# Optimization experiments

Hardware: AMD Instinct MI355X
Metric: run time of the kernel (lower is better)

Reference implementation:

```python
import jax, jax.numpy as jnp
import numpy as np


def _conv(x, w, b, pad):
    y = jax.lax.conv_general_dilated(x, w, (1, 1), [(pad, pad), (pad, pad)],
                                     dimension_numbers=('NCHW', 'OIHW', 'NCHW'))
    return y + b[None, :, None, None]


def _leaky(x):
    return jnp.where(x >= 0, x, 0.2 * x)


def _up_nearest(t, s):
    return jnp.repeat(jnp.repeat(t, s, axis=2), s, axis=3)


def _to_plane(d, dx, dy, size):
    # nearest-upsample d,dx,dy by `size` and add per-subpixel plane offsets
    c = jnp.linspace(-(size - 1) / 2, (size - 1) / 2, size).astype(d.dtype)
    H, W = d.shape[2], d.shape[3]
    a = jnp.tile(c, W)[None, None, None, :]   # x-offset pattern along width
    b = jnp.tile(c, H)[None, None, :, None]   # y-offset pattern along height
    return _up_nearest(d, size) + a * _up_nearest(dx, size) + b * _up_nearest(dy, size)


def _warp(x, disp):
    # grid_sample(x, grid) with grid = (xx - disp, yy), align_corners=True, zero padding.
    # y coords are exact integers, so this reduces to 1-D linear interp along W.
    B, C, H, W = x.shape
    ix = jnp.arange(W, dtype=x.dtype)[None, None, :] - disp[:, 0]  # [B,H,W]
    x0 = jnp.floor(ix)
    wx = ix - x0
    x0i = x0.astype(jnp.int32)
    x1i = x0i + 1
    ok0 = ((x0i >= 0) & (x0i < W)).astype(x.dtype)
    ok1 = ((x1i >= 0) & (x1i < W)).astype(x.dtype)

    def gather(idx):
        idx = jnp.clip(idx, 0, W - 1)
        return jnp.take_along_axis(x, jnp.broadcast_to(idx[:, None], (B, C, H, W)), axis=3)

    return ((1 - wx) * ok0)[:, None] * gather(x0i) + (wx * ok1)[:, None] * gather(x1i)


def _unshuffle(x, r=4):
    B, C, H, W = x.shape
    return x.reshape(B, C, H // r, r, W // r, r).transpose(0, 1, 3, 5, 2, 4).reshape(B, C * r * r, H // r, W // r)


def _tile_warping(tile_plane, fea_l, fea_r):
    d, dx, dy = tile_plane[:, 0:1], tile_plane[:, 1:2], tile_plane[:, 2:3]
    cvs = []
    for k in (-1.0, 0.0, 1.0):
        local_d = _to_plane(d + k, dx, dy, 4)
        cv = jnp.sum(jnp.abs(fea_l - _warp(fea_r, local_d)), axis=1, keepdims=True)
        cvs.append(_unshuffle(cv, 4))
    return jnp.concatenate(cvs, axis=1)


def _upsample_hyp(h, scale=2.0, size=2):
    d = _to_plane(h[:, 0:1], h[:, 1:2], h[:, 2:3], size) * scale
    rest = _up_nearest(h[:, 1:], size)
    return jnp.concatenate([d, rest], axis=1)


def _forward(fea_l, fea_r, cur, prev,
             w_dec, b_dec, w0, b0,
             w_r0c1, b_r0c1, w_r0c2, b_r0c2,
             w_r1c1, b_r1c1, w_r1c2, b_r1c2,
             w_last, b_last):
    fea = _unshuffle(jnp.sum(jnp.abs(fea_l), axis=1, keepdims=True), 4)  # [B,16,H/4,W/4]

    cur_cv = _tile_warping(cur[:, :3], fea_l, fea_r)
    cur_cv = _leaky(_conv(jnp.concatenate([fea, cur_cv], 1), w_dec, b_dec, 0))

    up_prev = _upsample_hyp(prev, 2.0, 2)
    prev_cv = _tile_warping(up_prev[:, :3], fea_l, fea_r)
    prev_cv = _leaky(_conv(jnp.concatenate([fea, prev_cv], 1), w_dec, b_dec, 0))

    aug = jnp.concatenate([cur, cur_cv, up_prev, prev_cv], 1)  # 64 ch
    h = _leaky(_conv(aug, w0, b0, 0))
    # resblock0 (BasicBlock + outer LeakyReLU)
    t = _leaky(_conv(h, w_r0c1, b_r0c1, 1))
    h = _leaky(_conv(t, w_r0c2, b_r0c2, 1) + h)
    # resblock1
    t = _leaky(_conv(h, w_r1c1, b_r1c1, 1))
    h = _leaky(_conv(t, w_r1c2, b_r1c2, 1) + h)
    u = _conv(h, w_last, b_last, 1)  # 34 ch

    conf = u[:, :2]
    prev_delta = u[:, 2:18]
    cur_delta = u[:, 18:34]
    mask = jnp.argmax(conf, axis=1, keepdims=True).astype(u.dtype)

    upd_cur = cur + cur_delta
    upd_cur = jnp.concatenate([jax.nn.relu(upd_cur[:, :1]), upd_cur[:, 1:]], 1)
    upd_prev = up_prev + prev_delta
    upd_prev = jnp.concatenate([jax.nn.relu(upd_prev[:, :1]), upd_prev[:, 1:]], 1)

    refined = mask * upd_cur + (1 - mask) * upd_prev
    return (refined,
            jnp.concatenate([upd_cur, conf[:, 1:2]], 1),
            jnp.concatenate([upd_prev, conf[:, :1]], 1))


def setup_inputs() -> dict:
    key = jax.random.key(0)
    ks = jax.random.split(key, 16)
    B, C, H, W = 2, 16, 384, 1280
    Ht, Wt = H // 4, W // 4
    inp = {
        'fea_l': jax.random.normal(ks[0], (B, C, H, W), jnp.float32),
        'fea_r': jax.random.normal(ks[1], (B, C, H, W), jnp.float32),
        'current_hypothesis': jax.random.uniform(ks[2], (B, 16, Ht, Wt), jnp.float32) * 4.0,
        'prev_hypothesis': jax.random.uniform(ks[3], (B, 16, Ht // 2, Wt // 2), jnp.float32) * 4.0,
    }
    s = 0.05
    inp['w_dec'] = jax.random.normal(ks[4], (16, 64, 1, 1), jnp.float32) * s
    inp['b_dec'] = jax.random.normal(ks[5], (16,), jnp.float32) * s
    inp['w0'] = jax.random.normal(ks[6], (32, 64, 1, 1), jnp.float32) * s
    inp['b0'] = jax.random.normal(ks[7], (32,), jnp.float32) * s
    inp['w_r0c1'] = jax.random.normal(ks[8], (32, 32, 3, 3), jnp.float32) * s
    inp['b_r0c1'] = jax.random.normal(ks[9], (32,), jnp.float32) * s
    inp['w_r0c2'] = jax.random.normal(ks[10], (32, 32, 3, 3), jnp.float32) * s
    inp['b_r0c2'] = jax.random.normal(ks[11], (32,), jnp.float32) * s
    inp['w_r1c1'] = jax.random.normal(ks[12], (32, 32, 3, 3), jnp.float32) * s
    inp['b_r1c1'] = jax.random.normal(ks[13], (32,), jnp.float32) * s
    inp['w_r1c2'] = jax.random.normal(ks[14], (32, 32, 3, 3), jnp.float32) * s
    inp['b_r1c2'] = jax.random.normal(ks[15], (32,), jnp.float32) * s
    k2 = jax.random.split(jax.random.key(1), 2)
    inp['w_last'] = jax.random.normal(k2[0], (34, 32, 3, 3), jnp.float32) * s
    inp['b_last'] = jax.random.normal(k2[1], (34,), jnp.float32) * s
    return inp


def reference(fea_l, fea_r, current_hypothesis, prev_hypothesis,
              w_dec, b_dec, w0, b0,
              w_r0c1, b_r0c1, w_r0c2, b_r0c2,
              w_r1c1, b_r1c1, w_r1c2, b_r1c2,
              w_last, b_last):
    return _forward(fea_l, fea_r, current_hypothesis, prev_hypothesis,
                    w_dec, b_dec, w0, b0,
                    w_r0c1, b_r0c1, w_r0c2, b_r0c2,
                    w_r1c1, b_r1c1, w_r1c2, b_r1c2,
                    w_last, b_last)
```

## Files before the change

kernel.cpp:

```cpp
#include <hip/hip_runtime.h>
#include <hip/hip_bf16.h>

#define B_ 2
#define C_ 16
#define H_ 384
#define W_ 1280
#define HT_ 96
#define WT_ 320
#define SP_ (HT_*WT_)
#define NPIX_ (B_*SP_)
#define HP_ 48
#define WP_ 160
#define SPP_ (HP_*WP_)

__device__ __forceinline__ float leaky(float v){ return v >= 0.f ? v : 0.2f*v; }

__global__ __launch_bounds__(256) void k_sentinel(float* __restrict__ out, int n, float v){
    int i = blockIdx.x*256 + threadIdx.x;
    if (i < n) out[i] = v;
}

__global__ __launch_bounds__(256) void k_warpfused(const float* __restrict__ cur,
        const float* __restrict__ prev,
        const float* __restrict__ fl, const float* __restrict__ fr,
        const float* __restrict__ wdec, const float* __restrict__ bdec,
        const float* __restrict__ w0, const float* __restrict__ b0,
        float* __restrict__ h){
    __shared__ float vc[16][65];
    __shared__ float vp[16][49];
    __shared__ float wl[64][16];
    __shared__ float inb[16][65];
    __shared__ float w0l[64][33];
    __shared__ float bl0[32];
    int tid = threadIdx.x;
    for (int i = tid; i < 1024; i += 256) wl[i>>4][i&15] = wdec[(i&15)*64 + (i>>4)];
    for (int i = tid; i < 2048; i += 256) w0l[i>>5][i&31] = w0[(i&31)*64 + (i>>5)];
    if (tid < 32) bl0[tid] = b0[tid];

    int tp  = tid >> 4;
    int sub = tid & 15;
    int yy = sub >> 2, xx = sub & 3;
    int ty = blockIdx.y;
    int tx0 = blockIdx.x*16;
    int tx = tx0 + tp;
    int b  = blockIdx.z;
    int y = ty*4 + yy, x = tx*4 + xx;

    {
        int ch = tid >> 4, px = tid & 15;
        int txp = tx0 + px;
        inb[px][ch] = cur[((size_t)(b*16 + ch)*HT_ + ty)*WT_ + txp];
        size_t pbase = ((size_t)(b*16)*HP_ + (ty>>1))*WP_ + (txp>>1);
        float v;
        if (ch == 0){
            float dv  = prev[pbase];
            float dxv = prev[pbase + SPP_];
            float dyv = prev[pbase + 2*SPP_];
            float cxs = (txp & 1) ? 0.5f : -0.5f;
            float cys = (ty  & 1) ? 0.5f : -0.5f;
            v = (dv + cxs*dxv + cys*dyv) * 2.0f;
        } else {
            v = prev[pbase + (size_t)ch*SPP_];
        }
        inb[px][32 + ch] = v;
    }

    size_t cb = ((size_t)(b*16)*HT_ + ty)*WT_ + tx;
    float dC  = cur[cb];
    float dxC = cur[cb + SP_];
    float dyC = cur[cb + 2*SP_];
    size_t pb = ((size_t)(b*16)*HP_ + (ty>>1))*WP_ + (tx>>1);
    float pd  = prev[pb];
    float pdx = prev[pb + SPP_];
    float pdy = prev[pb + 2*SPP_];
    float cxs = (tx & 1) ? 0.5f : -0.5f;
    float cys = (ty & 1) ? 0.5f : -0.5f;
    float dP  = (pd + cxs*pdx + cys*pdy) * 2.0f;

    const float c4[4] = {-1.5f,-0.5f,0.5f,1.5f};
    float ld0C = dC + c4[xx]*dxC + c4[yy]*dyC;
    float ld0P = dP + c4[xx]*pdx + c4[yy]*pdy;

    float wloC[4], whiC[4]; int xcC[4];
    {
        float ix  = (float)x - ld0C;
        float x0f = floorf(ix);
        float wx  = ix - x0f;
        int   x0  = (int)x0f;
        #pragma unroll
        for (int j = 0; j < 4; j++){
            int xi = x0 + (j-1);
            bool ok = (xi >= 0) && (xi < W_);
            xcC[j]  = xi < 0 ? 0 : (xi > W_-1 ? W_-1 : xi);
            wloC[j] = ok ? (1.f - wx) : 0.f;
            whiC[j] = ok ? wx : 0.f;
        }
    }
    float wloP[4], whiP[4]; int xcP[4];
    {
        float ix  = (float)x - ld0P;
        float x0f = floorf(ix);
        float wx  = ix - x0f;
        int   x0  = (int)x0f;
        #pragma unroll
        for (int j = 0; j < 4; j++){
            int xi = x0 + (j-1);
            bool ok = (xi >= 0) && (xi < W_);
            xcP[j]  = xi < 0 ? 0 : (xi > W_-1 ? W_-1 : xi);
            wloP[j] = ok ? (1.f - wx) : 0.f;
            whiP[j] = ok ? wx : 0.f;
        }
    }
    const float* plc = fl + (size_t)(b*C_)*H_*W_ + (size_t)y*W_ + x;
    const float* prr = fr + (size_t)(b*C_)*H_*W_ + (size_t)y*W_;
    float fsum=0.f, s0C=0.f, s1C=0.f, s2C=0.f, s0P=0.f, s1P=0.f, s2P=0.f;
    #pragma unroll 4
    for (int c = 0; c < C_; c++){
        const float* prc = prr + (size_t)c*H_*W_;
        float a  = plc[(size_t)c*H_*W_];
        float c0 = prc[xcC[0]];
        float c1 = prc[xcC[1]];
        float c2 = prc[xcC[2]];
        float c3 = prc[xcC[3]];
        float p0 = prc[xcP[0]];
        float p1 = prc[xcP[1]];
        float p2 = prc[xcP[2]];
        float p3 = prc[xcP[3]];
        fsum += fabsf(a);
        s0C += fabsf(a - (wloC[2]*c2 + whiC[3]*c3));
        s1C += fabsf(a - (wloC[1]*c1 + whiC[2]*c2));
        s2C += fabsf(a - (wloC[0]*c0 + whiC[1]*c1));
        s0P += fabsf(a - (wloP[2]*p2 + whiP[3]*p3));
        s1P += fabsf(a - (wloP[1]*p1 + whiP[2]*p2));
        s2P += fabsf(a - (wloP[0]*p0 + whiP[1]*p1));
    }
    vc[tp][sub]      = fsum;
    vc[tp][16 + sub] = s0C;
    vc[tp][32 + sub] = s1C;
    vc[tp][48 + sub] = s2C;
    vp[tp][sub]      = s0P;
    vp[tp][16 + sub] = s1P;
    vp[tp][32 + sub] = s2P;
    __syncthreads();

    {
        int oc  = tid >> 4;
        int tp2 = tid & 15;
        float common = 0.f, aC = 0.f, aP = 0.f;
        #pragma unroll 8
        for (int ic = 0; ic < 16; ic++) common += vc[tp2][ic] * wl[ic][oc];
        #pragma unroll 8
        for (int ic = 16; ic < 64; ic++){
            aC += vc[tp2][ic]      * wl[ic][oc];
            aP += vp[tp2][ic - 16] * wl[ic][oc];
        }
        float bb = bdec[oc];
        inb[tp2][16 + oc] = leaky(common + aC + bb);
        inb[tp2][48 + oc] = leaky(common + aP + bb);
    }
    __syncthreads();

    {
        int og = tid >> 4;
        int px = tid & 15;
        float acc0 = bl0[og];
        float acc1 = bl0[og + 16];
        #pragma unroll 8
        for (int ic = 0; ic < 64; ic++){
            float v = inb[px][ic];
            acc0 += v * w0l[ic][og];
            acc1 += v * w0l[ic][og + 16];
        }
        size_t hb = ((size_t)(b*32 + og)*HT_ + ty)*WT_ + tx0 + px;
        h[hb]              = leaky(acc0);
        h[hb + (size_t)16*HT_*WT_] = leaky(acc1);
    }
}

template<bool RES>
__global__ __launch_bounds__(256) void k_conv3(const float* __restrict__ in,
        const float* __restrict__ w, const float* __restrict__ bias,
        const float* res, float* out){
    __shared__ float it[8][6][34];
    __shared__ float wl[8][9][16];
    int tid = threadIdx.x;
    int gx = blockIdx.x*32, gy = blockIdx.y*4;
    int b     = blockIdx.z >> 1;
    int ocsel = blockIdx.z & 1;
    int ocg  = tid >> 6;
    int slot = tid & 63;
    int tx2  = (slot & 15)*2;
    int ty   = slot >> 4;
    float acc[4][2];
    #pragma unroll
    for (int o = 0; o < 4; o++)
        #pragma unroll
        for (int p = 0; p < 2; p++) acc[o][p] = 0.f;

    for (int ic0 = 0; ic0 < 32; ic0 += 8){
        for (int i = tid; i < 8*6*34; i += 256){
            int ic = i/(6*34); int r = i - ic*(6*34);
            int iy = r/34;     int ixx = r - iy*34;
            int ggy = gy + iy - 1, ggx = gx + ixx - 1;
            float v = 0.f;
            if (ggy >= 0 && ggy < HT_ && ggx >= 0 && ggx < WT_)
                v = in[((size_t)(b*32 + ic0+ic)*HT_ + ggy)*WT_ + ggx];
            it[ic][iy][ixx] = v;
        }
        for (int i = tid; i < 1152; i += 256){
            int ic = i/144; int r = i - ic*144;
            int kk = r >> 4; int ocl = r & 15;
            wl[ic][kk][ocl] = w[(size_t)((ocsel*16 + ocl)*32 + ic0+ic)*9 + kk];
        }
        __syncthreads();
        #pragma unroll
        for (int ic = 0; ic < 8; ic++){
            #pragma unroll
            for (int dy = 0; dy < 3; dy++){
                float inr[4];
                #pragma unroll
                for (int j = 0; j < 4; j++) inr[j] = it[ic][ty+dy][tx2+j];
                #pragma unroll
                for (int dx = 0; dx < 3; dx++){
                    const float4 wv = *(const float4*)(&wl[ic][dy*3+dx][ocg*4]);
                    const float wa[4] = {wv.x, wv.y, wv.z, wv.w};
                    #pragma unroll
                    for (int o = 0; o < 4; o++)
                        #pragma unroll
                        for (int p = 0; p < 2; p++)
                            acc[o][p] += inr[dx+p]*wa[o];
                }
            }
        }
        __syncthreads();
    }
    int oc0 = ocsel*16 + ocg*4;
    int yo = gy + ty;
    #pragma unroll
    for (int o = 0; o < 4; o++){
        float bo = bias[oc0+o];
        size_t ob = ((size_t)(b*32 + oc0+o)*HT_ + yo)*WT_ + gx + tx2;
        #pragma unroll
        for (int p = 0; p < 2; p++){
            float v = acc[o][p] + bo;
            if (RES) v += res[ob+p];
            out[ob+p] = leaky(v);
        }
    }
}

__global__ __launch_bounds__(256) void k_last(const float* __restrict__ in,
        const float* __restrict__ w, const float* __restrict__ bias,
        const float* __restrict__ cur, const float* __restrict__ prev,
        float* __restrict__ out){
    __shared__ float it[8][10][34];
    __shared__ float wl[8][9][36];
    __shared__ float bl[34];
    int tid = threadIdx.x;
    int gx = blockIdx.x*32, gy = blockIdx.y*8;
    int b = blockIdx.z;
    int tx = tid & 31, ty = tid >> 5;
    if (tid < 34) bl[tid] = bias[tid];
    float acc[34];
    #pragma unroll
    for (int o = 0; o < 34; o++) acc[o] = 0.f;

    for (int ic0 = 0; ic0 < 32; ic0 += 8){
        for (int i = tid; i < 8*10*34; i += 256){
            int ic = i/340; int r = i - ic*340;
            int iy = r/34;  int ixx = r - iy*34;
            int ggy = gy + iy - 1, ggx = gx + ixx - 1;
            float v = 0.f;
            if (ggy >= 0 && ggy < HT_ && ggx >= 0 && ggx < WT_)
                v = in[((size_t)(b*32 + ic0+ic)*HT_ + ggy)*WT_ + ggx];
            it[ic][iy][ixx] = v;
        }
        for (int i = tid; i < 8*9*34; i += 256){
            int ic = i/306; int r = i - ic*306;
            int kk = r/34;  int oc = r - kk*34;
            wl[ic][kk][oc] = w[(size_t)(oc*32 + ic0+ic)*9 + kk];
        }
        __syncthreads();
        for (int ic = 0; ic < 8; ic++){
            #pragma unroll
            for (int dy = 0; dy < 3; dy++){
                const float vv[3] = { it[ic][ty+dy][tx], it[ic][ty+dy][tx+1], it[ic][ty+dy][tx+2] };
                #pragma unroll
                for (int dx = 0; dx < 3; dx++){
                    const float* wp = &wl[ic][dy*3+dx][0];
                    float v = vv[dx];
                    #pragma unroll
                    for (int o = 0; o < 34; o++) acc[o] += v*wp[o];
                }
            }
        }
        __syncthreads();
    }
    int x = gx + tx, y = gy + ty;
    size_t pix = (size_t)y*WT_ + x;
    float conf0 = acc[0] + bl[0];
    float conf1 = acc[1] + bl[1];
    bool m = conf1 > conf0;
    size_t src = ((size_t)(b*16)*HP_ + (y>>1))*WP_ + (x>>1);
    float cx = (x & 1) ? 0.5f : -0.5f;
    float cy = (y & 1) ? 0.5f : -0.5f;
    const float* cp = cur + (size_t)b*16*SP_ + pix;
    float* o0 = out +               (size_t)b*16*SP_ + pix;
    float* o1 = out +  983040u  +   (size_t)b*17*SP_ + pix;
    float* o2 = out + 2027520u  +   (size_t)b*17*SP_ + pix;
    #pragma unroll
    for (int c = 0; c < 16; c++){
        float upv;
        if (c == 0){
            float dv  = prev[src];
            float dxv = prev[src + SPP_];
            float dyv = prev[src + 2*SPP_];
            upv = (dv + cx*dxv + cy*dyv) * 2.0f;
        } else {
            upv = prev[src + (size_t)c*SPP_];
        }
        float ucv = cp[(size_t)c*SP_] + acc[18+c] + bl[18+c];
        upv = upv + acc[2+c] + bl[2+c];
        if (c == 0){ ucv = fmaxf(ucv, 0.f); upv = fmaxf(upv, 0.f); }
        float rf = m ? ucv : upv;
        o0[(size_t)c*SP_] = rf;
        o1[(size_t)c*SP_] = ucv;
        o2[(size_t)c*SP_] = upv;
    }
    o1[(size_t)16*SP_] = conf1;
    o2[(size_t)16*SP_] = conf0;
}

#define WS_NEED (32u*NPIX_*4u)
#define OUT_ELEMS 3072000

extern "C" void kernel_launch(void* const* d_in, const int* in_sizes, int n_in,
                              void* d_out, int out_size, void* d_ws, size_t ws_size,
                              hipStream_t stream) {
    const float* fea_l  = (const float*)d_in[0];
    const float* fea_r  = (const float*)d_in[1];
    const float* cur    = (const float*)d_in[2];
    const float* prev   = (const float*)d_in[3];
    const float* w_dec  = (const float*)d_in[4];
    const float* b_dec  = (const float*)d_in[5];
    const float* w0     = (const float*)d_in[6];
    const float* b0     = (const float*)d_in[7];
    const float* w_r0c1 = (const float*)d_in[8];
    const float* b_r0c1 = (const float*)d_in[9];
    const float* w_r0c2 = (const float*)d_in[10];
    const float* b_r0c2 = (const float*)d_in[11];
    const float* w_r1c1 = (const float*)d_in[12];
    const float* b_r1c1 = (const float*)d_in[13];
    const float* w_r1c2 = (const float*)d_in[14];
    const float* b_r1c2 = (const float*)d_in[15];
    const float* w_last = (const float*)d_in[16];
    const float* b_last = (const float*)d_in[17];

    float* out = (float*)d_out;

    if (ws_size < (size_t)WS_NEED){
        k_sentinel<<<(OUT_ELEMS+255)/256, 256, 0, stream>>>(out, OUT_ELEMS, (float)(ws_size >> 10));
        return;
    }

    float* h = (float*)d_ws;
    float* t = out;

    dim3 gw(20, 96, 2);
    k_warpfused<<<gw, 256, 0, stream>>>(cur, prev, fea_l, fea_r, w_dec, b_dec, w0, b0, h);

    dim3 g3(10, 24, 4);
    k_conv3<false><<<g3, 256, 0, stream>>>(h, w_r0c1, b_r0c1, nullptr, t);
    k_conv3<true> <<<g3, 256, 0, stream>>>(t, w_r0c2, b_r0c2, h, h);
    k_conv3<false><<<g3, 256, 0, stream>>>(h, w_r1c1, b_r1c1, nullptr, t);
    k_conv3<true> <<<g3, 256, 0, stream>>>(t, w_r1c2, b_r1c2, h, h);

    dim3 gl(10, 12, 2);
    k_last<<<gl, 256, 0, stream>>>(h, w_last, b_last, cur, prev, out);
}
```

Baseline: 453.7 us.

## Stage right-feature rows in LDS for warp cost volume and double-buffer conv tiles

The fused warp kernel computes the block's min/max gather column with shared-memory atomics. When that span fits in 256 columns, it stages the needed fl/fr rows into a shared-memory pool in groups of 4 channels instead of doing scattered global gathers per channel. The weight and input loads for the decoder are moved after the cost loop so they can reuse the same pool. The conv3 and last-conv kernels switch to double-buffered shared tiles, with the row pitch padded to 35, so the next channel group loads while the current one computes. This adds shared memory, more synchronisation, and a fallback path for wide spans.

```diff
diff --git a/kernel.cpp b/kernel.cpp
--- a/kernel.cpp
+++ b/kernel.cpp
@@ -28,15 +28,16 @@
         float* __restrict__ h){
     __shared__ float vc[16][65];
     __shared__ float vp[16][49];
-    __shared__ float wl[64][16];
-    __shared__ float inb[16][65];
-    __shared__ float w0l[64][33];
-    __shared__ float bl0[32];
+    __shared__ int   s_red[2];
+    __shared__ float upool[5152];
+    float (*flA)[4][65]  = (float(*)[4][65])(upool);
+    float (*frW)[4][257] = (float(*)[4][257])(upool + 1040);
+    float (*wlp)[16]     = (float(*)[16])(upool);
+    float (*inb)[65]     = (float(*)[65])(upool + 1024);
+    float (*w0l)[33]     = (float(*)[33])(upool + 2064);
+    float *bl0           = upool + 4176;
+
     int tid = threadIdx.x;
-    for (int i = tid; i < 1024; i += 256) wl[i>>4][i&15] = wdec[(i&15)*64 + (i>>4)];
-    for (int i = tid; i < 2048; i += 256) w0l[i>>5][i&31] = w0[(i&31)*64 + (i>>5)];
-    if (tid < 32) bl0[tid] = b0[tid];
-
     int tp  = tid >> 4;
     int sub = tid & 15;
     int yy = sub >> 2, xx = sub & 3;
@@ -46,24 +47,7 @@
     int b  = blockIdx.z;
     int y = ty*4 + yy, x = tx*4 + xx;
 
-    {
-        int ch = tid >> 4, px = tid & 15;
-        int txp = tx0 + px;
-        inb[px][ch] = cur[((size_t)(b*16 + ch)*HT_ + ty)*WT_ + txp];
-        size_t pbase = ((size_t)(b*16)*HP_ + (ty>>1))*WP_ + (txp>>1);
-        float v;
-        if (ch == 0){
-            float dv  = prev[pbase];
-            float dxv = prev[pbase + SPP_];
-            float dyv = prev[pbase + 2*SPP_];
-            float cxs = (txp & 1) ? 0.5f : -0.5f;
-            float cys = (ty  & 1) ? 0.5f : -0.5f;
-            v = (dv + cxs*dxv + cys*dyv) * 2.0f;
-        } else {
-            v = prev[pbase + (size_t)ch*SPP_];
-        }
-        inb[px][32 + ch] = v;
-    }
+    if (tid == 0){ s_red[0] = 0x7fffffff; s_red[1] = -0x7fffffff; }
 
     size_t cb = ((size_t)(b*16)*HT_ + ty)*WT_ + tx;
     float dC  = cur[cb];
@@ -111,29 +95,79 @@
             whiP[j] = ok ? wx : 0.f;
         }
     }
-    const float* plc = fl + (size_t)(b*C_)*H_*W_ + (size_t)y*W_ + x;
-    const float* prr = fr + (size_t)(b*C_)*H_*W_ + (size_t)y*W_;
+    __syncthreads();
+    atomicMin(&s_red[0], min(xcC[0], xcP[0]));
+    atomicMax(&s_red[1], max(xcC[3], xcP[3]));
+    __syncthreads();
+    int wmn   = s_red[0];
+    int wspan = s_red[1] - wmn + 1;
+
+    const size_t HW = (size_t)H_*W_;
     float fsum=0.f, s0C=0.f, s1C=0.f, s2C=0.f, s0P=0.f, s1P=0.f, s2P=0.f;
-    #pragma unroll 4
-    for (int c = 0; c < C_; c++){
-        const float* prc = prr + (size_t)c*H_*W_;
-        float a  = plc[(size_t)c*H_*W_];
-        float c0 = prc[xcC[0]];
-        float c1 = prc[xcC[1]];
-        float c2 = prc[xcC[2]];
-        float c3 = prc[xcC[3]];
-        float p0 = prc[xcP[0]];
-        float p1 = prc[xcP[1]];
-        float p2 = prc[xcP[2]];
-        float p3 = prc[xcP[3]];
-        fsum += fabsf(a);
-        s0C += fabsf(a - (wloC[2]*c2 + whiC[3]*c3));
-        s1C += fabsf(a - (wloC[1]*c1 + whiC[2]*c2));
-        s2C += fabsf(a - (wloC[0]*c0 + whiC[1]*c1));
-        s0P += fabsf(a - (wloP[2]*p2 + whiP[3]*p3));
-        s1P += fabsf(a - (wloP[1]*p1 + whiP[2]*p2));
-        s2P += fabsf(a - (wloP[0]*p0 + whiP[1]*p1));
-    }
+
+    if (wspan <= 256){
+        int W64 = (wspan + 63) & ~63;
+        int o0C = xcC[0]-wmn, o1C = xcC[1]-wmn, o2C = xcC[2]-wmn, o3C = xcC[3]-wmn;
+        int o0P = xcP[0]-wmn, o1P = xcP[1]-wmn, o2P = xcP[2]-wmn, o3P = xcP[3]-wmn;
+        int y0 = ty*4, xb = tx0*4;
+        int pxl = tp*4 + xx;
+        for (int c0 = 0; c0 < 16; c0 += 4){
+            for (int i = tid; i < 1024; i += 256){
+                int ci = i >> 8, r = (i >> 6) & 3, px = i & 63;
+                flA[ci][r][px] = fl[(size_t)(b*C_ + c0+ci)*HW + (size_t)(y0+r)*W_ + xb + px];
+            }
+            for (int ci = 0; ci < 4; ci++){
+                const float* base = fr + (size_t)(b*C_ + c0+ci)*HW;
+                for (int r = 0; r < 4; r++){
+                    const float* rowp = base + (size_t)(y0+r)*W_;
+                    for (int px = tid; px < W64; px += 256){
+                        int gx = wmn + px;
+                        frW[ci][r][px] = (gx < W_) ? rowp[gx] : 0.f;
+                    }
+                }
+            }
+            __syncthreads();
+            #pragma unroll
+            for (int ci = 0; ci < 4; ci++){
+                float a = flA[ci][yy][pxl];
+                const float* row = &frW[ci][yy][0];
+                float c0v = row[o0C], c1v = row[o1C], c2v = row[o2C], c3v = row[o3C];
+                float p0v = row[o0P], p1v = row[o1P], p2v = row[o2P], p3v = row[o3P];
+                fsum += fabsf(a);
+                s0C += fabsf(a - (wloC[2]*c2v + whiC[3]*c3v));
+                s1C += fabsf(a - (wloC[1]*c1v + whiC[2]*c2v));
+                s2C += fabsf(a - (wloC[0]*c0v + whiC[1]*c1v));
+                s0P += fabsf(a - (wloP[2]*p2v + whiP[3]*p3v));
+                s1P += fabsf(a - (wloP[1]*p1v + whiP[2]*p2v));
+                s2P += fabsf(a - (wloP[0]*p0v + whiP[1]*p1v));
+            }
+            __syncthreads();
+        }
+    } else {
+        const float* plc = fl + (size_t)(b*C_)*HW + (size_t)y*W_ + x;
+        const float* prr = fr + (size_t)(b*C_)*HW + (size_t)y*W_;
+        #pragma unroll 4
+        for (int c = 0; c < C_; c++){
+            const float* prc = prr + (size_t)c*HW;
+            float a  = plc[(size_t)c*HW];
+            float c0v = prc[xcC[0]];
+            float c1v = prc[xcC[1]];
+            float c2v = prc[xcC[2]];
+            float c3v = prc[xcC[3]];
+            float p0v = prc[xcP[0]];
+            float p1v = prc[xcP[1]];
+            float p2v = prc[xcP[2]];
+            float p3v = prc[xcP[3]];
+            fsum += fabsf(a);
+            s0C += fabsf(a - (wloC[2]*c2v + whiC[3]*c3v));
+            s1C += fabsf(a - (wloC[1]*c1v + whiC[2]*c2v));
+            s2C += fabsf(a - (wloC[0]*c0v + whiC[1]*c1v));
+            s0P += fabsf(a - (wloP[2]*p2v + whiP[3]*p3v));
+            s1P += fabsf(a - (wloP[1]*p1v + whiP[2]*p2v));
+            s2P += fabsf(a - (wloP[0]*p0v + whiP[1]*p1v));
+        }
+    }
+
     vc[tp][sub]      = fsum;
     vc[tp][16 + sub] = s0C;
     vc[tp][32 + sub] = s1C;
@@ -141,6 +175,28 @@
     vp[tp][sub]      = s0P;
     vp[tp][16 + sub] = s1P;
     vp[tp][32 + sub] = s2P;
+
+    for (int i = tid; i < 1024; i += 256) wlp[i>>4][i&15] = wdec[(i&15)*64 + (i>>4)];
+    for (int i = tid; i < 2048; i += 256) w0l[i>>5][i&31] = w0[(i&31)*64 + (i>>5)];
+    if (tid < 32) bl0[tid] = b0[tid];
+    {
+        int ch = tid >> 4, px = tid & 15;
+        int txp = tx0 + px;
+        inb[px][ch] = cur[((size_t)(b*16 + ch)*HT_ + ty)*WT_ + txp];
+        size_t pbase = ((size_t)(b*16)*HP_ + (ty>>1))*WP_ + (txp>>1);
+        float v;
+        if (ch == 0){
+            float dv  = prev[pbase];
+            float dxv = prev[pbase + SPP_];
+            float dyv = prev[pbase + 2*SPP_];
+            float cx2 = (txp & 1) ? 0.5f : -0.5f;
+            float cy2 = (ty  & 1) ? 0.5f : -0.5f;
+            v = (dv + cx2*dxv + cy2*dyv) * 2.0f;
+        } else {
+            v = prev[pbase + (size_t)ch*SPP_];
+        }
+        inb[px][32 + ch] = v;
+    }
     __syncthreads();
 
     {
@@ -148,11 +204,11 @@
         int tp2 = tid & 15;
         float common = 0.f, aC = 0.f, aP = 0.f;
         #pragma unroll 8
-        for (int ic = 0; ic < 16; ic++) common += vc[tp2][ic] * wl[ic][oc];
+        for (int ic = 0; ic < 16; ic++) common += vc[tp2][ic] * wlp[ic][oc];
         #pragma unroll 8
         for (int ic = 16; ic < 64; ic++){
-            aC += vc[tp2][ic]      * wl[ic][oc];
-            aP += vp[tp2][ic - 16] * wl[ic][oc];
+            aC += vc[tp2][ic]      * wlp[ic][oc];
+            aP += vp[tp2][ic - 16] * wlp[ic][oc];
         }
         float bb = bdec[oc];
         inb[tp2][16 + oc] = leaky(common + aC + bb);
@@ -172,7 +228,7 @@
             acc1 += v * w0l[ic][og + 16];
         }
         size_t hb = ((size_t)(b*32 + og)*HT_ + ty)*WT_ + tx0 + px;
-        h[hb]              = leaky(acc0);
+        h[hb]                      = leaky(acc0);
         h[hb + (size_t)16*HT_*WT_] = leaky(acc1);
     }
 }
@@ -181,12 +237,33 @@
 __global__ __launch_bounds__(256) void k_conv3(const float* __restrict__ in,
         const float* __restrict__ w, const float* __restrict__ bias,
         const float* res, float* out){
-    __shared__ float it[8][6][34];
-    __shared__ float wl[8][9][16];
+    __shared__ float it[2][8][6][35];
+    __shared__ float wl[2][8][9][16];
     int tid = threadIdx.x;
     int gx = blockIdx.x*32, gy = blockIdx.y*4;
     int b     = blockIdx.z >> 1;
     int ocsel = blockIdx.z & 1;
+
+    auto stage = [&](int buf, int ic0){
+        for (int i = tid; i < 8*6*34; i += 256){
+            int ic = i/204; int r = i - ic*204;
+            int iy = r/34;  int ixx = r - iy*34;
+            int ggy = gy + iy - 1, ggx = gx + ixx - 1;
+            float v = 0.f;
+            if (ggy >= 0 && ggy < HT_ && ggx >= 0 && ggx < WT_)
+                v = in[((size_t)(b*32 + ic0+ic)*HT_ + ggy)*WT_ + ggx];
+            it[buf][ic][iy][ixx] = v;
+        }
+        for (int i = tid; i < 1152; i += 256){
+            int ic = i/144; int r = i - ic*144;
+            int kk = r >> 4; int ocl = r & 15;
+            wl[buf][ic][kk][ocl] = w[(size_t)((ocsel*16 + ocl)*32 + ic0+ic)*9 + kk];
+        }
+    };
+
+    stage(0, 0);
+    __syncthreads();
+
     int ocg  = tid >> 6;
     int slot = tid & 63;
     int tx2  = (slot & 15)*2;
@@ -197,32 +274,19 @@
         #pragma unroll
         for (int p = 0; p < 2; p++) acc[o][p] = 0.f;
 
-    for (int ic0 = 0; ic0 < 32; ic0 += 8){
-        for (int i = tid; i < 8*6*34; i += 256){
-            int ic = i/(6*34); int r = i - ic*(6*34);
-            int iy = r/34;     int ixx = r - iy*34;
-            int ggy = gy + iy - 1, ggx = gx + ixx - 1;
-            float v = 0.f;
-            if (ggy >= 0 && ggy < HT_ && ggx >= 0 && ggx < WT_)
-                v = in[((size_t)(b*32 + ic0+ic)*HT_ + ggy)*WT_ + ggx];
-            it[ic][iy][ixx] = v;
-        }
-        for (int i = tid; i < 1152; i += 256){
-            int ic = i/144; int r = i - ic*144;
-            int kk = r >> 4; int ocl = r & 15;
-            wl[ic][kk][ocl] = w[(size_t)((ocsel*16 + ocl)*32 + ic0+ic)*9 + kk];
-        }
-        __syncthreads();
+    for (int ph = 0; ph < 4; ph++){
+        int cb = ph & 1;
+        if (ph < 3) stage(cb ^ 1, (ph+1)*8);
         #pragma unroll
         for (int ic = 0; ic < 8; ic++){
             #pragma unroll
             for (int dy = 0; dy < 3; dy++){
                 float inr[4];
                 #pragma unroll
-                for (int j = 0; j < 4; j++) inr[j] = it[ic][ty+dy][tx2+j];
+                for (int j = 0; j < 4; j++) inr[j] = it[cb][ic][ty+dy][tx2+j];
                 #pragma unroll
                 for (int dx = 0; dx < 3; dx++){
-                    const float4 wv = *(const float4*)(&wl[ic][dy*3+dx][ocg*4]);
+                    const float4 wv = *(const float4*)(&wl[cb][ic][dy*3+dx][ocg*4]);
                     const float wa[4] = {wv.x, wv.y, wv.z, wv.w};
                     #pragma unroll
                     for (int o = 0; o < 4; o++)
@@ -253,19 +317,16 @@
         const float* __restrict__ w, const float* __restrict__ bias,
         const float* __restrict__ cur, const float* __restrict__ prev,
         float* __restrict__ out){
-    __shared__ float it[8][10][34];
-    __shared__ float wl[8][9][36];
+    __shared__ float it[2][8][10][35];
+    __shared__ float wl[2][8][9][36];
     __shared__ float bl[34];
     int tid = threadIdx.x;
     int gx = blockIdx.x*32, gy = blockIdx.y*8;
     int b = blockIdx.z;
     int tx = tid & 31, ty = tid >> 5;
     if (tid < 34) bl[tid] = bias[tid];
-    float acc[34];
-    #pragma unroll
-    for (int o = 0; o < 34; o++) acc[o] = 0.f;
-
-    for (int ic0 = 0; ic0 < 32; ic0 += 8){
+
+    auto stage = [&](int buf, int ic0){
         for (int i = tid; i < 8*10*34; i += 256){
             int ic = i/340; int r = i - ic*340;
             int iy = r/34;  int ixx = r - iy*34;
@@ -273,21 +334,31 @@
             float v = 0.f;
             if (ggy >= 0 && ggy < HT_ && ggx >= 0 && ggx < WT_)
                 v = in[((size_t)(b*32 + ic0+ic)*HT_ + ggy)*WT_ + ggx];
-            it[ic][iy][ixx] = v;
+            it[buf][ic][iy][ixx] = v;
         }
         for (int i = tid; i < 8*9*34; i += 256){
             int ic = i/306; int r = i - ic*306;
             int kk = r/34;  int oc = r - kk*34;
-            wl[ic][kk][oc] = w[(size_t)(oc*32 + ic0+ic)*9 + kk];
-        }
-        __syncthreads();
+            wl[buf][ic][kk][oc] = w[(size_t)(oc*32 + ic0+ic)*9 + kk];
+        }
+    };
+
+    float acc[34];
+    #pragma unroll
+    for (int o = 0; o < 34; o++) acc[o] = 0.f;
+
+    stage(0, 0);
+    __syncthreads();
+    for (int ph = 0; ph < 4; ph++){
+        int cb = ph & 1;
+        if (ph < 3) stage(cb ^ 1, (ph+1)*8);
         for (int ic = 0; ic < 8; ic++){
             #pragma unroll
             for (int dy = 0; dy < 3; dy++){
-                const float vv[3] = { it[ic][ty+dy][tx], it[ic][ty+dy][tx+1], it[ic][ty+dy][tx+2] };
+                const float vv[3] = { it[cb][ic][ty+dy][tx], it[cb][ic][ty+dy][tx+1], it[cb][ic][ty+dy][tx+2] };
                 #pragma unroll
                 for (int dx = 0; dx < 3; dx++){
-                    const float* wp = &wl[ic][dy*3+dx][0];
+                    const float* wp = &wl[cb][ic][dy*3+dx][0];
                     float v = vv[dx];
                     #pragma unroll
                     for (int o = 0; o < 34; o++) acc[o] += v*wp[o];
```

Result: slower. 605.9 us (+33.5%).
